# Kernel optimization log

Measured on AMD Instinct MI355X. Metric: run time of the kernel, lower is better.

## Reference

```python
import jax, jax.numpy as jnp
import numpy as np
from jax import lax

N = 200000
CIN = 64
COUT = 128
K = 27  # 3^3 kernel offsets
EPS = 1e-5


def _make_rulebook(key, n, k):
    ki, km = jax.random.split(key)
    idx = jax.random.randint(ki, (k, n), 0, n, dtype=jnp.int32)
    keep = jax.random.uniform(km, (k, n)) < 0.5
    idx = jnp.where(keep, idx, -1)
    # center offset is always the voxel itself (submanifold conv)
    idx = idx.at[k // 2].set(jnp.arange(n, dtype=jnp.int32))
    return idx


def setup_inputs() -> dict:
    key = jax.random.key(0)
    ks = jax.random.split(key, 8)
    feats = jax.random.normal(ks[0], (N, CIN), dtype=jnp.float32)
    nbr1 = _make_rulebook(ks[1], N, K)
    nbr2 = _make_rulebook(ks[2], N, K)
    W1 = jax.random.normal(ks[3], (K, CIN, COUT), dtype=jnp.float32) * 0.05
    W2 = jax.random.normal(ks[4], (K, COUT, COUT), dtype=jnp.float32) * 0.05
    Wd = jax.random.normal(ks[5], (CIN, COUT), dtype=jnp.float32) * 0.05
    g1 = jnp.ones((COUT,), jnp.float32); b1 = jnp.zeros((COUT,), jnp.float32)
    g2 = jnp.ones((COUT,), jnp.float32); b2 = jnp.zeros((COUT,), jnp.float32)
    gd = jnp.ones((COUT,), jnp.float32); bd = jnp.zeros((COUT,), jnp.float32)
    return dict(feats=feats, nbr1=nbr1, nbr2=nbr2, W1=W1, W2=W2, Wd=Wd,
                g1=g1, b1=b1, g2=g2, b2=b2, gd=gd, bd=bd)


def sparse_conv(feats, W, nbr):
    """Rulebook sparse conv: gather neighbors per offset, GEMM, accumulate.
    feats: [N, Cin]; W: [K, Cin, Cout]; nbr: [K, N] int (-1 = missing)."""
    n = feats.shape[0]
    acc0 = jnp.zeros((n, W.shape[-1]), feats.dtype)

    def body(acc, xs):
        idx, Wk = xs  # [N], [Cin, Cout]
        valid = (idx >= 0).astype(feats.dtype)[:, None]
        g = feats[jnp.clip(idx, 0)] * valid  # masked gather [N, Cin]
        return acc + g @ Wk, None

    out, _ = lax.scan(body, acc0, (nbr, W))
    return out


def batchnorm(x, gamma, beta):
    mean = jnp.mean(x, axis=0)
    var = jnp.var(x, axis=0)
    return (x - mean) * lax.rsqrt(var + EPS) * gamma + beta


def reference(feats, nbr1, nbr2, W1, W2, Wd, g1, b1, g2, b2, gd, bd):
    h = sparse_conv(feats, W1, nbr1)
    h = jax.nn.relu(batchnorm(h, g1, b1))
    h = sparse_conv(h, W2, nbr2)
    h = batchnorm(h, g2, b2)
    skip = batchnorm(feats @ Wd, gd, bd)  # 1x1 conv downsample (Cin != Cout)
    return jax.nn.relu(h + skip)
```

## Files before the change

kernel.cpp:

```cpp
#include <hip/hip_runtime.h>
#include <stdint.h>

#define KOFF 27
#define CIN 64
#define COUT 128
#define EPS 1e-5f

using frag_ab = __attribute__((ext_vector_type(8))) short;
using frag_cd = __attribute__((ext_vector_type(4))) float;

__device__ __forceinline__ float bf2f(unsigned short u) {
  union { unsigned int i; float f; } x; x.i = ((unsigned int)u) << 16; return x.f;
}
__device__ __forceinline__ unsigned short f2bf(float f) {
  union { float f; unsigned int i; } x; x.f = f;
  unsigned int u = x.i;
  u += 0x7fffu + ((u >> 16) & 1u);
  return (unsigned short)(u >> 16);
}

__device__ __forceinline__ void gld16(const void* gptr, void* lptr) {
  __builtin_amdgcn_global_load_lds(
      (const __attribute__((address_space(1))) unsigned int*)gptr,
      (__attribute__((address_space(3))) unsigned int*)lptr, 16, 0, 0);
}

template <int CI, bool GATHER, bool OF32>
__global__ __launch_bounds__(256, 4) void conv_kernel(
    const unsigned short* __restrict__ X, const int* __restrict__ nbr,
    const unsigned short* __restrict__ Wt, void* __restrict__ Yv,
    const unsigned short* __restrict__ zpage, float* __restrict__ sums,
    int n, int koff) {
  constexpr int NC = CI / 32;
  __shared__ unsigned short Alds[3][128 * 32];
  __shared__ unsigned short Blds[2][4096];

  const int tid = threadIdx.x;
  const int lane = tid & 63;
  const int wave = tid >> 6;
  const int row0 = blockIdx.x * 128;
  const int wrow = (wave >> 1) * 64;
  const int wcol = (wave & 1) * 64;
  const int m = lane & 15;
  const int q = lane >> 4;
  const int srow0 = wave * 16 + (lane >> 2);
  const int sl = lane & 3;

  frag_cd acc[4][4];
#pragma unroll
  for (int i = 0; i < 4; ++i)
#pragma unroll
    for (int j = 0; j < 4; ++j) acc[i][j] = (frag_cd){0.f, 0.f, 0.f, 0.f};

  int idxc[2], idxn[2];

  auto load_idx = [&](int ko, int (&dst)[2]) {
#pragma unroll
    for (int i = 0; i < 2; ++i) {
      const int grow = row0 + srow0 + i * 64;
      int v = -1;
      if (grow < n) v = GATHER ? nbr[(size_t)ko * n + grow] : grow;
      dst[i] = v;
    }
  };
  auto stageA = [&](int buf, int kc, const int (&idx)[2]) {
#pragma unroll
    for (int i = 0; i < 2; ++i) {
      const int row = srow0 + i * 64;
      const int g = sl ^ ((row >> 1) & 3);
      const unsigned short* ga =
          (idx[i] >= 0) ? X + (size_t)idx[i] * CI + kc * 32 + g * 8 : zpage;
      gld16(ga, &Alds[buf][(i * 64 + wave * 16) * 32]);
    }
  };
  auto stageB = [&](int buf, int t) {
    const unsigned short* base = Wt + (size_t)t * 4096;
#pragma unroll
    for (int c = 0; c < 2; ++c) {
      const int chunk = c * 4 + wave;
      gld16(base + (size_t)chunk * 512 + lane * 8, &Blds[buf][chunk * 512]);
    }
  };
  auto do_mfma = [&](int abuf, int bbuf) {
    frag_ab a[4];
#pragma unroll
    for (int i = 0; i < 4; ++i) {
      const int row = wrow + 16 * i + m;
      a[i] = *(const frag_ab*)(&Alds[abuf][row * 32 + (q ^ ((row >> 1) & 3)) * 8]);
    }
    frag_ab b[4];
#pragma unroll
    for (int j = 0; j < 4; ++j)
      b[j] = *(const frag_ab*)(&Blds[bbuf][q * 1024 + (wcol + 16 * j + m) * 8]);
#pragma unroll
    for (int i = 0; i < 4; ++i)
#pragma unroll
      for (int j = 0; j < 4; ++j)
        acc[i][j] = __builtin_amdgcn_mfma_f32_16x16x32_bf16(a[i], b[j],
                                                            acc[i][j], 0, 0, 0);
  };

  const int T = koff * NC;
  load_idx(0, idxc);
  if (koff > 1) load_idx(1, idxn);
  stageA(0, 0, idxc);
  stageB(0, 0);
  stageA(1, 1, idxc);

  int bufc = 0;
  for (int t = 0; t < T - 1; ++t) {
    asm volatile("s_waitcnt vmcnt(2)" ::: "memory");
    __builtin_amdgcn_s_barrier();
    const int s = t + 2;
    if (GATHER && s < T) {
      const int kos = s / NC;
      if ((s & (NC - 1)) == 0) {
        idxc[0] = idxn[0];
        idxc[1] = idxn[1];
        if (kos + 1 < koff) load_idx(kos + 1, idxn);
      }
    }
    const int u = t + 1;
    stageB(u & 1, u);
    if (s < T) {
      int bufs = bufc + 2; if (bufs >= 3) bufs -= 3;
      stageA(bufs, s & (NC - 1), idxc);
    }
    do_mfma(bufc, t & 1);
    if (++bufc == 3) bufc = 0;
  }
  asm volatile("s_waitcnt vmcnt(0)" ::: "memory");
  __builtin_amdgcn_s_barrier();
  do_mfma(bufc, (T - 1) & 1);

#pragma unroll
  for (int j = 0; j < 4; ++j) {
    float s = 0.f, qq = 0.f;
#pragma unroll
    for (int i = 0; i < 4; ++i)
#pragma unroll
      for (int r = 0; r < 4; ++r) {
        float v = acc[i][j][r];
        s += v; qq += v * v;
      }
    s += __shfl_xor(s, 16); s += __shfl_xor(s, 32);
    qq += __shfl_xor(qq, 16); qq += __shfl_xor(qq, 32);
    if (lane < 16) {
      const int col = wcol + 16 * j + lane;
      atomicAdd(&sums[col], s);
      atomicAdd(&sums[COUT + col], qq);
    }
  }

#pragma unroll
  for (int i = 0; i < 4; ++i) {
#pragma unroll
    for (int r = 0; r < 4; ++r) {
      const int grow = row0 + wrow + 16 * i + q * 4 + r;
      if (grow < n) {
#pragma unroll
        for (int j = 0; j < 4; ++j) {
          const int gcol = wcol + 16 * j + m;
          if (OF32)
            ((float*)Yv)[(size_t)grow * COUT + gcol] = acc[i][j][r];
          else
            ((unsigned short*)Yv)[(size_t)grow * COUT + gcol] = f2bf(acc[i][j][r]);
        }
      }
    }
  }
}

__global__ __launch_bounds__(256, 2) void convskip_kernel(
    const float* __restrict__ feats, const float* __restrict__ Wd,
    unsigned short* __restrict__ featsb, unsigned short* __restrict__ sX,
    float* __restrict__ sums, int n) {
  __shared__ unsigned short Alds[2][128 * 32];
  const int tid = threadIdx.x;
  const int lane = tid & 63;
  const int wave = tid >> 6;
  const int row0 = blockIdx.x * 128;
  const int wrow = (wave >> 1) * 64;
  const int wcol = (wave & 1) * 64;
  const int m = lane & 15;
  const int q = lane >> 4;

#pragma unroll
  for (int c = 0; c < 4; ++c) {
    int u = c * 256 + tid;
    int kc = u >> 9;
    int v = u & 511;
    int row = v >> 2;
    int s = v & 3;
    int g = s ^ ((row >> 1) & 3);
    int grow = row0 + row;
    uint4 out = make_uint4(0u, 0u, 0u, 0u);
    if (grow < n) {
      const float* p = feats + (size_t)grow * 64 + kc * 32 + g * 8;
      float4 lo = *(const float4*)p;
      float4 hi = *(const float4*)(p + 4);
      out.x = (unsigned)f2bf(lo.x) | ((unsigned)f2bf(lo.y) << 16);
      out.y = (unsigned)f2bf(lo.z) | ((unsigned)f2bf(lo.w) << 16);
      out.z = (unsigned)f2bf(hi.x) | ((unsigned)f2bf(hi.y) << 16);
      out.w = (unsigned)f2bf(hi.z) | ((unsigned)f2bf(hi.w) << 16);
      *(uint4*)(featsb + (size_t)grow * 64 + kc * 32 + g * 8) = out;
    }
    *(uint4*)(&Alds[kc][row * 32 + s * 8]) = out;
  }
  __syncthreads();

  frag_cd acc[4][4];
#pragma unroll
  for (int i = 0; i < 4; ++i)
#pragma unroll
    for (int j = 0; j < 4; ++j) acc[i][j] = (frag_cd){0.f, 0.f, 0.f, 0.f};

#pragma unroll
  for (int kc = 0; kc < 2; ++kc) {
    frag_ab b[4];
#pragma unroll
    for (int j = 0; j < 4; ++j) {
      const int co = wcol + 16 * j + m;
#pragma unroll
      for (int e = 0; e < 8; ++e)
        b[j][e] = (short)f2bf(Wd[(size_t)(kc * 32 + q * 8 + e) * 128 + co]);
    }
    frag_ab a[4];
#pragma unroll
    for (int i = 0; i < 4; ++i) {
      const int row = wrow + 16 * i + m;
      a[i] = *(const frag_ab*)(&Alds[kc][row * 32 + (q ^ ((row >> 1) & 3)) * 8]);
    }
#pragma unroll
    for (int i = 0; i < 4; ++i)
#pragma unroll
      for (int j = 0; j < 4; ++j)
        acc[i][j] = __builtin_amdgcn_mfma_f32_16x16x32_bf16(a[i], b[j],
                                                            acc[i][j], 0, 0, 0);
  }

#pragma unroll
  for (int j = 0; j < 4; ++j) {
    float s = 0.f, qq = 0.f;
#pragma unroll
    for (int i = 0; i < 4; ++i)
#pragma unroll
      for (int r = 0; r < 4; ++r) {
        float v = acc[i][j][r];
        s += v; qq += v * v;
      }
    s += __shfl_xor(s, 16); s += __shfl_xor(s, 32);
    qq += __shfl_xor(qq, 16); qq += __shfl_xor(qq, 32);
    if (lane < 16) {
      const int col = wcol + 16 * j + lane;
      atomicAdd(&sums[col], s);
      atomicAdd(&sums[COUT + col], qq);
    }
  }

#pragma unroll
  for (int i = 0; i < 4; ++i) {
#pragma unroll
    for (int r = 0; r < 4; ++r) {
      const int grow = row0 + wrow + 16 * i + q * 4 + r;
      if (grow < n) {
#pragma unroll
        for (int j = 0; j < 4; ++j)
          sX[(size_t)grow * COUT + wcol + 16 * j + m] = f2bf(acc[i][j][r]);
      }
    }
  }
}

__global__ void prep_kernel(const float* __restrict__ W1,
                            const float* __restrict__ W2,
                            unsigned short* __restrict__ Wt1,
                            unsigned short* __restrict__ Wt2,
                            float* __restrict__ zbase,
                            float* __restrict__ zpage) {
  const int NZ = 768 + 64;
  const int NW1 = KOFF * CIN * 128;
  const int NW2 = KOFF * COUT * 128;
  int gid = blockIdx.x * 256 + threadIdx.x;
  if (gid < NZ) {
    if (gid < 768) zbase[gid] = 0.f; else zpage[gid - 768] = 0.f;
    return;
  }
  gid -= NZ;
  const float* src;
  unsigned short* dst;
  int ci;
  if (gid < NW1) { src = W1; dst = Wt1; ci = CIN; }
  else if (gid < NW1 + NW2) { gid -= NW1; src = W2; dst = Wt2; ci = COUT; }
  else return;
  int e = gid & 7;
  int co = (gid >> 3) & 127;
  int qq = (gid >> 10) & 3;
  int slab = gid >> 12;
  int nc = ci >> 5;
  int ko = slab / nc;
  int kc = slab - ko * nc;
  int cin = kc * 32 + qq * 8 + e;
  dst[gid] = f2bf(src[((size_t)ko * ci + cin) * 128 + co]);
}

__global__ void norm_relu_kernel(unsigned short* __restrict__ x,
                                 const float* __restrict__ sums,
                                 const float* __restrict__ gamma,
                                 const float* __restrict__ beta,
                                 int n, int total8) {
  __shared__ float sc[COUT], sh[COUT];
  const int tid = threadIdx.x;
  if (tid < COUT) {
    float inv_n = 1.f / (float)n;
    float mean = sums[tid] * inv_n;
    float var = sums[COUT + tid] * inv_n - mean * mean;
    float s = gamma[tid] * rsqrtf(var + EPS);
    sc[tid] = s;
    sh[tid] = beta[tid] - mean * s;
  }
  __syncthreads();
  int gid = blockIdx.x * 256 + tid;
  if (gid >= total8) return;
  size_t i = (size_t)gid * 8;
  int c0 = (int)(i & 127);
  uint4 v = *(const uint4*)(x + i);
  unsigned int w[4] = {v.x, v.y, v.z, v.w};
  unsigned int wo[4];
#pragma unroll
  for (int e = 0; e < 4; ++e) {
    int c = c0 + 2 * e;
    float f0 = bf2f((unsigned short)(w[e] & 0xffffu));
    float f1 = bf2f((unsigned short)(w[e] >> 16));
    f0 = fmaxf(f0 * sc[c] + sh[c], 0.f);
    f1 = fmaxf(f1 * sc[c + 1] + sh[c + 1], 0.f);
    wo[e] = (unsigned int)f2bf(f0) | ((unsigned int)f2bf(f1) << 16);
  }
  *(uint4*)(x + i) = make_uint4(wo[0], wo[1], wo[2], wo[3]);
}

__global__ void final_kernel(float* __restrict__ h2,
                             const unsigned short* __restrict__ s,
                             const float* __restrict__ sums2,
                             const float* __restrict__ sumsd,
                             const float* __restrict__ g2,
                             const float* __restrict__ b2,
                             const float* __restrict__ gd,
                             const float* __restrict__ bd,
                             int n, int total4) {
  __shared__ float sc2[COUT], sh2[COUT], scd[COUT], shd[COUT];
  const int tid = threadIdx.x;
  if (tid < COUT) {
    float inv_n = 1.f / (float)n;
    float mean = sums2[tid] * inv_n;
    float var = sums2[COUT + tid] * inv_n - mean * mean;
    float sa = g2[tid] * rsqrtf(var + EPS);
    sc2[tid] = sa;
    sh2[tid] = b2[tid] - mean * sa;
    mean = sumsd[tid] * inv_n;
    var = sumsd[COUT + tid] * inv_n - mean * mean;
    float sb = gd[tid] * rsqrtf(var + EPS);
    scd[tid] = sb;
    shd[tid] = bd[tid] - mean * sb;
  }
  __syncthreads();
  int gid = blockIdx.x * 256 + tid;
  if (gid >= total4) return;
  size_t i = (size_t)gid * 4;
  int c = (int)(i & 127);
  float4 a = *(const float4*)(h2 + i);
  uint2 sv = *(const uint2*)(s + i);
  float b0 = bf2f((unsigned short)(sv.x & 0xffffu));
  float b1 = bf2f((unsigned short)(sv.x >> 16));
  float b2f = bf2f((unsigned short)(sv.y & 0xffffu));
  float b3 = bf2f((unsigned short)(sv.y >> 16));
  float4 o;
  o.x = fmaxf(a.x * sc2[c] + sh2[c] + b0 * scd[c] + shd[c], 0.f);
  o.y = fmaxf(a.y * sc2[c + 1] + sh2[c + 1] + b1 * scd[c + 1] + shd[c + 1], 0.f);
  o.z = fmaxf(a.z * sc2[c + 2] + sh2[c + 2] + b2f * scd[c + 2] + shd[c + 2], 0.f);
  o.w = fmaxf(a.w * sc2[c + 3] + sh2[c + 3] + b3 * scd[c + 3] + shd[c + 3], 0.f);
  *(float4*)(h2 + i) = o;
}

extern "C" void kernel_launch(void* const* d_in, const int* in_sizes, int n_in,
                              void* d_out, int out_size, void* d_ws,
                              size_t ws_size, hipStream_t stream) {
  (void)n_in; (void)out_size; (void)ws_size;
  const float* feats = (const float*)d_in[0];
  const int* nbr1 = (const int*)d_in[1];
  const int* nbr2 = (const int*)d_in[2];
  const float* W1 = (const float*)d_in[3];
  const float* W2 = (const float*)d_in[4];
  const float* Wd = (const float*)d_in[5];
  const float* g1 = (const float*)d_in[6];
  const float* b1 = (const float*)d_in[7];
  const float* g2 = (const float*)d_in[8];
  const float* b2 = (const float*)d_in[9];
  const float* gd = (const float*)d_in[10];
  const float* bd = (const float*)d_in[11];

  const int n = in_sizes[0] / CIN;

  char* ws = (char*)d_ws;
  unsigned short* Wt1 = (unsigned short*)(ws);
  unsigned short* Wt2 = (unsigned short*)(ws + 442368);
  unsigned short* h1 = (unsigned short*)(ws + 1343488);
  unsigned short* sX = (unsigned short*)(ws + 52543488);
  float* sums1 = (float*)(ws + 103743488);
  float* sums2 = sums1 + 2 * COUT;
  float* sumsd = sums1 + 4 * COUT;
  unsigned short* zpage = (unsigned short*)(ws + 103743488 + 8192);

  float* h2 = (float*)d_out;
  unsigned short* featsb = (unsigned short*)((char*)d_out + 76800000);

  const int prep_units = (768 + 64) + KOFF * CIN * 128 + KOFF * COUT * 128;
  prep_kernel<<<(prep_units + 255) / 256, 256, 0, stream>>>(
      W1, W2, Wt1, Wt2, sums1, (float*)zpage);

  const int mblocks = (n + 127) / 128;
  convskip_kernel<<<mblocks, 256, 0, stream>>>(feats, Wd, featsb, sX, sumsd, n);

  conv_kernel<CIN, true, false><<<mblocks, 256, 0, stream>>>(
      featsb, nbr1, Wt1, h1, zpage, sums1, n, KOFF);

  const int total8 = n * COUT / 8;
  norm_relu_kernel<<<(total8 + 255) / 256, 256, 0, stream>>>(h1, sums1, g1, b1, n, total8);

  conv_kernel<COUT, true, true><<<mblocks, 256, 0, stream>>>(
      h1, nbr2, Wt2, h2, zpage, sums2, n, KOFF);

  const int total4 = n * COUT / 4;
  final_kernel<<<(total4 + 255) / 256, 256, 0, stream>>>(
      h2, sX, sums2, sumsd, g2, b2, gd, bd, n, total4);
}
```

Measured before the change: 685.5 us.

## Restructure conv pipeline to K=64 steps with B fragments loaded directly from global

Reworks the main loop of the sparse conv kernel. Each step now stages a 128x64 A tile (double-buffered with an XOR swizzle) instead of 128x32 (triple-buffered). Weight fragments are read straight from global into registers instead of through LDS, and a full __syncthreads replaces the partial vmcnt wait. Launch bounds drop from 4 to 3 blocks per CU. This halves the number of barriers and removes the B-tile LDS traffic, but it adds register pressure and exposes global-load latency on B, and it weakens the overlap because A is only double-buffered.

```diff
diff --git a/kernel.cpp b/kernel.cpp
--- a/kernel.cpp
+++ b/kernel.cpp
@@ -26,14 +26,13 @@
 }
 
 template <int CI, bool GATHER, bool OF32>
-__global__ __launch_bounds__(256, 4) void conv_kernel(
+__global__ __launch_bounds__(256, 3) void conv_kernel(
     const unsigned short* __restrict__ X, const int* __restrict__ nbr,
     const unsigned short* __restrict__ Wt, void* __restrict__ Yv,
     const unsigned short* __restrict__ zpage, float* __restrict__ sums,
     int n, int koff) {
-  constexpr int NC = CI / 32;
-  __shared__ unsigned short Alds[3][128 * 32];
-  __shared__ unsigned short Blds[2][4096];
+  constexpr int SUB = CI / 64;
+  __shared__ unsigned short Alds[2][128 * 64];
 
   const int tid = threadIdx.x;
   const int lane = tid & 63;
@@ -43,8 +42,6 @@
   const int wcol = (wave & 1) * 64;
   const int m = lane & 15;
   const int q = lane >> 4;
-  const int srow0 = wave * 16 + (lane >> 2);
-  const int sl = lane & 3;
 
   frag_cd acc[4][4];
 #pragma unroll
@@ -52,86 +49,81 @@
 #pragma unroll
     for (int j = 0; j < 4; ++j) acc[i][j] = (frag_cd){0.f, 0.f, 0.f, 0.f};
 
-  int idxc[2], idxn[2];
-
-  auto load_idx = [&](int ko, int (&dst)[2]) {
-#pragma unroll
-    for (int i = 0; i < 2; ++i) {
-      const int grow = row0 + srow0 + i * 64;
+  frag_ab b[2][4];
+  int idxc[4];
+
+  auto load_idx = [&](int ko, int (&dst)[4]) {
+#pragma unroll
+    for (int c = 0; c < 4; ++c) {
+      const int grow = row0 + wave * 32 + c * 8 + (lane >> 3);
       int v = -1;
       if (grow < n) v = GATHER ? nbr[(size_t)ko * n + grow] : grow;
-      dst[i] = v;
+      dst[c] = v;
     }
   };
-  auto stageA = [&](int buf, int kc, const int (&idx)[2]) {
-#pragma unroll
-    for (int i = 0; i < 2; ++i) {
-      const int row = srow0 + i * 64;
-      const int g = sl ^ ((row >> 1) & 3);
+  auto stageA = [&](int buf, const int (&idx)[4], int sub) {
+    const int cho = sub * 64 + ((lane & 7) ^ (lane >> 3)) * 8;
+#pragma unroll
+    for (int c = 0; c < 4; ++c) {
       const unsigned short* ga =
-          (idx[i] >= 0) ? X + (size_t)idx[i] * CI + kc * 32 + g * 8 : zpage;
-      gld16(ga, &Alds[buf][(i * 64 + wave * 16) * 32]);
+          (idx[c] >= 0) ? X + (size_t)idx[c] * CI + cho : zpage;
+      gld16(ga, &Alds[buf][(wave * 32 + c * 8) * 64]);
     }
   };
-  auto stageB = [&](int buf, int t) {
-    const unsigned short* base = Wt + (size_t)t * 4096;
-#pragma unroll
-    for (int c = 0; c < 2; ++c) {
-      const int chunk = c * 4 + wave;
-      gld16(base + (size_t)chunk * 512 + lane * 8, &Blds[buf][chunk * 512]);
+  auto loadB = [&](int t) {
+#pragma unroll
+    for (int kk = 0; kk < 2; ++kk) {
+      const unsigned short* base =
+          Wt + (size_t)(2 * t + kk) * 4096 + q * 1024 + m * 8;
+#pragma unroll
+      for (int j = 0; j < 4; ++j)
+        b[kk][j] = *(const frag_ab*)(base + (wcol + 16 * j) * 8);
     }
   };
-  auto do_mfma = [&](int abuf, int bbuf) {
-    frag_ab a[4];
-#pragma unroll
-    for (int i = 0; i < 4; ++i) {
-      const int row = wrow + 16 * i + m;
-      a[i] = *(const frag_ab*)(&Alds[abuf][row * 32 + (q ^ ((row >> 1) & 3)) * 8]);
-    }
-    frag_ab b[4];
-#pragma unroll
-    for (int j = 0; j < 4; ++j)
-      b[j] = *(const frag_ab*)(&Blds[bbuf][q * 1024 + (wcol + 16 * j + m) * 8]);
-#pragma unroll
-    for (int i = 0; i < 4; ++i)
-#pragma unroll
-      for (int j = 0; j < 4; ++j)
-        acc[i][j] = __builtin_amdgcn_mfma_f32_16x16x32_bf16(a[i], b[j],
-                                                            acc[i][j], 0, 0, 0);
+  auto do_mfma = [&](int abuf) {
+#pragma unroll
+    for (int kk = 0; kk < 2; ++kk) {
+      frag_ab a[4];
+#pragma unroll
+      for (int i = 0; i < 4; ++i) {
+        const int row = wrow + 16 * i + m;
+        a[i] = *(const frag_ab*)(
+            &Alds[abuf][row * 64 + ((kk * 4 + q) ^ (m & 7)) * 8]);
+      }
+#pragma unroll
+      for (int i = 0; i < 4; ++i)
+#pragma unroll
+        for (int j = 0; j < 4; ++j)
+          acc[i][j] = __builtin_amdgcn_mfma_f32_16x16x32_bf16(
+              a[i], b[kk][j], acc[i][j], 0, 0, 0);
+    }
   };
 
-  const int T = koff * NC;
-  load_idx(0, idxc);
-  if (koff > 1) load_idx(1, idxn);
-  stageA(0, 0, idxc);
-  stageB(0, 0);
-  stageA(1, 1, idxc);
-
-  int bufc = 0;
-  for (int t = 0; t < T - 1; ++t) {
-    asm volatile("s_waitcnt vmcnt(2)" ::: "memory");
-    __builtin_amdgcn_s_barrier();
-    const int s = t + 2;
-    if (GATHER && s < T) {
-      const int kos = s / NC;
-      if ((s & (NC - 1)) == 0) {
-        idxc[0] = idxn[0];
-        idxc[1] = idxn[1];
-        if (kos + 1 < koff) load_idx(kos + 1, idxn);
-      }
-    }
+  const int T = koff * SUB;
+  {
+    int idx0[4];
+    load_idx(0, idx0);
+    stageA(0, idx0, 0);
+    if (SUB == 2) {
+#pragma unroll
+      for (int c = 0; c < 4; ++c) idxc[c] = idx0[c];
+    } else {
+      load_idx(1, idxc);
+    }
+  }
+
+  for (int t = 0; t < T; ++t) {
+    __syncthreads();
     const int u = t + 1;
-    stageB(u & 1, u);
-    if (s < T) {
-      int bufs = bufc + 2; if (bufs >= 3) bufs -= 3;
-      stageA(bufs, s & (NC - 1), idxc);
-    }
-    do_mfma(bufc, t & 1);
-    if (++bufc == 3) bufc = 0;
-  }
-  asm volatile("s_waitcnt vmcnt(0)" ::: "memory");
-  __builtin_amdgcn_s_barrier();
-  do_mfma(bufc, (T - 1) & 1);
+    if (u < T) {
+      stageA(u & 1, idxc, (SUB == 2) ? (u & 1) : 0);
+      const int w2 = t + 2;
+      if (w2 < T && (SUB == 1 || (w2 & 1) == 0))
+        load_idx((SUB == 2) ? (w2 >> 1) : w2, idxc);
+    }
+    loadB(t);
+    do_mfma(t & 1);
+  }
 
 #pragma unroll
   for (int j = 0; j < 4; ++j) {
```

Result: faster. 664.7 us (-3.0%).
